# Optimization experiments

Measured on AMD Instinct MI355X. Metric: run time of the kernel, lower is better.

Reference implementation:

```python
import jax, jax.numpy as jnp
import numpy as np

B, T, NCH, NBIN, NBAND = 2, 400, 8, 512, 40
NPV = NCH * NCH


def setup_inputs() -> dict:
    key = jax.random.key(0)
    ks = jax.random.split(key, 7)
    bins_real = jax.random.normal(ks[0], (B, T, NCH, NBIN), jnp.float32)
    bins_imag = jax.random.normal(ks[1], (B, T, NCH, NBIN), jnp.float32)
    band_matrix_real = jax.random.normal(ks[2], (NBIN, NBAND), jnp.float32) * 0.05
    band_matrix_imag = jax.random.normal(ks[3], (NBIN, NBAND), jnp.float32) * 0.05
    cov_to_pv_real = jax.random.normal(ks[4], (NPV, NCH * NCH), jnp.float32) * 0.1
    cov_to_pv_imag = jax.random.normal(ks[5], (NPV, NCH * NCH), jnp.float32) * 0.1
    tau = jax.random.uniform(ks[6], (NBAND,), jnp.float32, 0.8, 0.99)
    return {
        'bins_real': bins_real, 'bins_imag': bins_imag,
        'band_matrix_real': band_matrix_real, 'band_matrix_imag': band_matrix_imag,
        'cov_to_pv_real': cov_to_pv_real, 'cov_to_pv_imag': cov_to_pv_imag,
        'tau': tau,
    }


def _power_vector(bins_real, bins_imag, band_matrix_real, band_matrix_imag,
                  cov_to_pv_real, cov_to_pv_imag, tau):
    x = jax.lax.complex(bins_real, bins_imag)            # (B,T,C,F)
    nch = x.shape[-2]
    EPS = 1e-20
    # per-bin covariance outer product, flattened cov dim: (B,T,F,C*C)
    cov = jnp.einsum('btif,btjf->btfij', x, jnp.conj(x))
    b, t, f = cov.shape[:3]
    cov = cov.reshape(b, t, f, nch * nch)
    diag = jnp.arange(nch) * (nch + 1)                   # diagonal indices in cov dim
    trace = jnp.clip(jnp.sum(cov.real[..., diag], axis=-1, keepdims=True), EPS, None)
    cov = cov / trace                                    # per-bin trace normalisation
    # phase adjustment along the bin axis (n=1 -> lag of 2 bins)
    c = jnp.swapaxes(cov, -1, -2)                        # (B,T,C2,F)
    prod = jnp.conj(c[..., :-2]) * c[..., 2:]
    ang = jnp.arctan2(prod.imag, prod.real)
    ang = jnp.concatenate([ang[..., :1], ang, ang[..., -1:]], axis=-1)  # edge pad
    adj = jnp.abs(c) * jax.lax.complex(jnp.cos(ang), jnp.sin(ang))
    adj = adj.at[..., diag, :].set(c[..., diag, :])      # keep original diagonals
    # band projection: contract bins against (F,K) band matrix
    bm = jax.lax.complex(band_matrix_real, band_matrix_imag)
    band_cov = jnp.einsum('btcf,fk->btkc', adj, bm)      # (B,T,K,C2)
    dsum = jnp.clip(band_cov.real[..., diag].sum(-1, keepdims=True), EPS, None)
    band_cov = band_cov / dsum
    # first-order IIR smoothing over frames, per-band pole tau
    a = tau[:, None].astype(band_cov.real.dtype)         # (K,1)
    def step(carry, xt):
        y = a * carry + (1.0 - a) * xt
        return y, y
    y0 = jnp.zeros_like(band_cov[:, 0])                  # (B,K,C2)
    _, ys = jax.lax.scan(step, y0, jnp.moveaxis(band_cov, 1, 0))
    band_cov = jnp.moveaxis(ys, 0, 1)                    # (B,T,K,C2)
    # cov -> power vector projection, real part
    c2p = jax.lax.complex(cov_to_pv_real, cov_to_pv_imag)  # (P,C2)
    pv = jnp.einsum('pc,btkc->btkp', c2p, band_cov).real   # (B,T,K,P)
    return pv


def reference(bins_real, bins_imag, band_matrix_real, band_matrix_imag,
              cov_to_pv_real, cov_to_pv_imag, tau):
    return _power_vector(bins_real, bins_imag, band_matrix_real, band_matrix_imag,
                         cov_to_pv_real, cov_to_pv_imag, tau)
```

## Files before the change

### kernel.cpp

```cpp
#include <hip/hip_runtime.h>

#define B_    2
#define T_    400
#define NCH_  8
#define NBIN_ 512
#define NBAND_ 40
#define NPV_  64

using short8  = __attribute__((ext_vector_type(8))) short;
using float4v = __attribute__((ext_vector_type(4))) float;

static __device__ inline unsigned pkbf(float x, float y) {
  union { float f; unsigned u; } a, b;
  a.f = x; b.f = y;
  unsigned ra = a.u + 0x7fffu + ((a.u >> 16) & 1u);
  unsigned rb = b.u + 0x7fffu + ((b.u >> 16) & 1u);
  return (ra >> 16) | (rb & 0xffff0000u);
}
static __device__ inline void upk(unsigned u, float& lo, float& hi) {
  union { unsigned q; float f; } a, b;
  a.q = u << 16; b.q = u & 0xffff0000u;
  lo = a.f; hi = b.f;
}
static __device__ inline unsigned swapvar(unsigned u) {
  unsigned r = u ^ 0x80000000u;
  return (r >> 16) | (r << 16);
}
static __device__ inline void gld_lds16(const uint4* g, uint4* l) {
  auto* lds_ptr = reinterpret_cast<__attribute__((address_space(3))) uint4*>(
      reinterpret_cast<uintptr_t>(l));
  auto* g_ptr = reinterpret_cast<const __attribute__((address_space(1))) uint4*>(
      reinterpret_cast<uintptr_t>(g));
  __builtin_amdgcn_global_load_lds(g_ptr, lds_ptr, 16, 0, 0);
}

__global__ __launch_bounds__(256) void pv_prep(
    const float* __restrict__ bmr, const float* __restrict__ bmi,
    const float* __restrict__ c2pr, const float* __restrict__ c2pi,
    float* __restrict__ ws)
{
  const int tid = threadIdx.x;
  const int blk = blockIdx.x;
  if (blk == 0) {
    __shared__ float sds[256];
    int k = tid & 63, part = tid >> 6;
    float s = 0.f;
    if (k < NBAND_) {
      const float* col = bmr + k;
      #pragma unroll 16
      for (int f = part * 128; f < part * 128 + 128; f++) s += col[f * 40];
    }
    sds[tid] = s;
    __syncthreads();
    if (tid < NBAND_) {
      float t = sds[tid] + sds[tid + 64] + sds[tid + 128] + sds[tid + 192];
      ws[tid] = 1.0f / fmaxf(t, 1e-20f);
    }
  } else if (blk <= 24) {
    int F = (blk - 1) * 256 + tid;
    int l = F & 63;
    int fid = F >> 6;
    int s5 = fid / 3;
    int n = fid - s5 * 3;
    int k = n * 16 + (l & 15);
    int quad = l >> 4;
    unsigned dw[4];
    #pragma unroll
    for (int t2 = 0; t2 < 4; t2++) {
      float v0 = 0.f, v1 = 0.f;
      if (k < NBAND_) {
        int f = s5 * 16 + quad * 4 + t2;
        v0 = bmr[f * 40 + k]; v1 = bmi[f * 40 + k];
      }
      dw[t2] = pkbf(v0, v1);
    }
    ((uint4*)((char*)ws + 1024))[F] = make_uint4(dw[0], dw[1], dw[2], dw[3]);
  } else {
    int F2 = (blk - 25) * 256 + tid;
    int lane = F2 & 63, E = F2 >> 6;
    int nt = E >> 2, ks = E & 3;
    int n = lane & 15, quad = lane >> 4;
    int p = nt * 16 + n;
    unsigned dw[4];
    #pragma unroll
    for (int t2 = 0; t2 < 4; t2++) {
      int c = ks * 16 + quad * 4 + t2;
      dw[t2] = pkbf(c2pr[p * 64 + c], -c2pi[p * 64 + c]);
    }
    ((uint4*)((char*)ws + 197632))[E * 64 + lane] = make_uint4(dw[0], dw[1], dw[2], dw[3]);
  }
}

__global__ __launch_bounds__(256, 4) void pv_main(
    const float* __restrict__ br, const float* __restrict__ bi,
    const float* __restrict__ ws, float* __restrict__ out)
{
  __shared__ __align__(16) unsigned smem[10240];
  unsigned* vsh = smem;
  uint4*    bst = (uint4*)(smem + 4096);

  const int bt  = blockIdx.x;
  const int tid = threadIdx.x;
  const float* pr  = br + (size_t)bt * (NCH_ * NBIN_);
  const float* pim = bi + (size_t)bt * (NCH_ * NBIN_);

  const int mt   = tid >> 6;
  const int lane = tid & 63;
  const int m16  = lane & 15;
  const int quad = lane >> 4;
  const int p    = mt * 16 + m16;
  const int ich  = p >> 3, jch = p & 7;
  const uint4* BF0 = (const uint4*)((const char*)ws + 1024);

  {
    const uint4* g = BF0 + tid;
    uint4* l = bst + tid;
    gld_lds16(g, l);
    gld_lds16(g + 256, l + 256);
    gld_lds16(g + 512, l + 512);
  }

  #pragma unroll
  for (int fs = 0; fs < 2; fs++) {
    const int f = fs * 256 + tid;
    const int fm = (f == 0) ? 0 : ((f == 511) ? 509 : f - 1);
    const int fp = (f == 0) ? 2 : ((f == 511) ? 511 : f + 1);
    float tr = 0.f;
    float t1[8], t2[8];
    #pragma unroll
    for (int c = 0; c < 8; c++) {
      const float* cr = pr + c * 512;
      const float* ci = pim + c * 512;
      float xr = cr[f],   xi = ci[f];
      float xrm = cr[fm], xim = ci[fm];
      float xrp = cr[fp], xip = ci[fp];
      tr = fmaf(xr, xr, tr); tr = fmaf(xi, xi, tr);
      float Gr = fmaf(xrm, xrp,  xim * xip);
      float Gi = fmaf(xrm, xip, -(xim * xrp));
      float am = fmaxf(fmaxf(fabsf(Gr), fabsf(Gi)), 1e-30f);
      float rc = __builtin_amdgcn_rcpf(am);
      float q1 = Gr * rc, q2 = Gi * rc;
      float n2 = fmaf(q1, q1, q2 * q2);
      float rn = __builtin_amdgcn_rsqf(n2);
      bool ok = n2 > 0.f;
      float ur = ok ? q1 * rn : 1.f;
      float ui = ok ? q2 * rn : 0.f;
      float mg = __builtin_amdgcn_sqrtf(fmaf(xr, xr, xi * xi));
      t1[c] = mg * ur; t2[c] = mg * ui;
    }
    float scv = __builtin_amdgcn_rsqf(fmaxf(tr, 1e-20f));
    #pragma unroll
    for (int c = 0; c < 8; c++)
      vsh[c * 512 + f] = pkbf(t1[c] * scv, t2[c] * scv);
  }
  __syncthreads();

  const uint4* Avp = (const uint4*)(vsh + ich * 512) + quad;
  const uint4* Bvp = (const uint4*)(vsh + jch * 512) + quad;

  float4v acc[6];
  #pragma unroll
  for (int g = 0; g < 6; g++) acc[g] = (float4v){0.f, 0.f, 0.f, 0.f};

  for (int st = 0; st < 8; st++) {
    if (st < 7) {
      const uint4* g = BF0 + (st + 1) * 768 + tid;
      uint4* l = bst + ((st + 1) & 1) * 768 + tid;
      gld_lds16(g, l);
      gld_lds16(g + 256, l + 256);
      gld_lds16(g + 512, l + 512);
    }
    const uint4* bb = bst + (st & 1) * 768;
    #pragma unroll
    for (int q = 0; q < 4; q++) {
      const int s = st * 4 + q;
      uint4 av = Avp[s * 4];
      uint4 bv = Bvp[s * 4];
      uint4 cb0 = bb[(q * 3 + 0) * 64 + lane];
      uint4 cb1 = bb[(q * 3 + 1) * 64 + lane];
      uint4 cb2 = bb[(q * 3 + 2) * 64 + lane];
      float ar[4], ai[4];
      {
        float vr, vi, wr, wi;
        upk(av.x, vr, vi); upk(bv.x, wr, wi);
        ar[0] = fmaf(vr, wr,  vi * wi); ai[0] = fmaf(vi, wr, -(vr * wi));
        upk(av.y, vr, vi); upk(bv.y, wr, wi);
        ar[1] = fmaf(vr, wr,  vi * wi); ai[1] = fmaf(vi, wr, -(vr * wi));
        upk(av.z, vr, vi); upk(bv.z, wr, wi);
        ar[2] = fmaf(vr, wr,  vi * wi); ai[2] = fmaf(vi, wr, -(vr * wi));
        upk(av.w, vr, vi); upk(bv.w, wr, wi);
        ar[3] = fmaf(vr, wr,  vi * wi); ai[3] = fmaf(vi, wr, -(vr * wi));
      }
      uint4 au1 = make_uint4(pkbf(ar[0], -ai[0]), pkbf(ar[1], -ai[1]),
                             pkbf(ar[2], -ai[2]), pkbf(ar[3], -ai[3]));
      uint4 au2 = make_uint4(swapvar(au1.x), swapvar(au1.y),
                             swapvar(au1.z), swapvar(au1.w));
      short8 af1 = __builtin_bit_cast(short8, au1);
      short8 af2 = __builtin_bit_cast(short8, au2);
      short8 b0 = __builtin_bit_cast(short8, cb0);
      short8 b1 = __builtin_bit_cast(short8, cb1);
      short8 b2 = __builtin_bit_cast(short8, cb2);
      acc[0] = __builtin_amdgcn_mfma_f32_16x16x32_bf16(af1, b0, acc[0], 0, 0, 0);
      acc[3] = __builtin_amdgcn_mfma_f32_16x16x32_bf16(af2, b0, acc[3], 0, 0, 0);
      acc[1] = __builtin_amdgcn_mfma_f32_16x16x32_bf16(af1, b1, acc[1], 0, 0, 0);
      acc[4] = __builtin_amdgcn_mfma_f32_16x16x32_bf16(af2, b1, acc[4], 0, 0, 0);
      acc[2] = __builtin_amdgcn_mfma_f32_16x16x32_bf16(af1, b2, acc[2], 0, 0, 0);
      acc[5] = __builtin_amdgcn_mfma_f32_16x16x32_bf16(af2, b2, acc[5], 0, 0, 0);
    }
    __syncthreads();
  }

  const uint4* EF = ((const uint4*)((const char*)ws + 197632)) + (mt * 4) * 64 + lane;
  uint4 eb[4];
  #pragma unroll
  for (int ks = 0; ks < 4; ks++) eb[ks] = EF[ks * 64];

  unsigned* bcsh = smem;
  #pragma unroll
  for (int n = 0; n < 3; n++) {
    uint4 w4 = make_uint4(pkbf(acc[n][0], acc[n + 3][0]),
                          pkbf(acc[n][1], acc[n + 3][1]),
                          pkbf(acc[n][2], acc[n + 3][2]),
                          pkbf(acc[n][3], acc[n + 3][3]));
    *(uint4*)(bcsh + (n * 16 + m16) * 68 + mt * 16 + quad * 4) = w4;
  }
  __syncthreads();

  float4v eacc[3];
  #pragma unroll
  for (int kt = 0; kt < 3; kt++) eacc[kt] = (float4v){0.f, 0.f, 0.f, 0.f};
  #pragma unroll
  for (int ks = 0; ks < 4; ks++) {
    short8 bfr = __builtin_bit_cast(short8, eb[ks]);
    #pragma unroll
    for (int kt = 0; kt < 3; kt++) {
      uint4 a4 = *(const uint4*)(bcsh + (kt * 16 + m16) * 68 + ks * 16 + quad * 4);
      short8 afr = __builtin_bit_cast(short8, a4);
      eacc[kt] = __builtin_amdgcn_mfma_f32_16x16x32_bf16(afr, bfr, eacc[kt], 0, 0, 0);
    }
  }
  float* op = out + (size_t)bt * (NBAND_ * NPV_);
  const float4* wsd = (const float4*)ws;
  #pragma unroll
  for (int kt = 0; kt < 3; kt++) {
    float4 dv = wsd[kt * 4 + quad];
    float dva[4] = {dv.x, dv.y, dv.z, dv.w};
    #pragma unroll
    for (int r = 0; r < 4; r++) {
      int k = kt * 16 + quad * 4 + r;
      if (k < NBAND_)
        op[k * 64 + mt * 16 + m16] = eacc[kt][r] * dva[r];
    }
  }
}

__global__ __launch_bounds__(256) void pv_iir3(float* __restrict__ z,
                                               const float* __restrict__ tau)
{
  __shared__ float gsh[16][16];
  const int pg = blockIdx.x & 3;
  const int bk = blockIdx.x >> 2;
  const int k = bk % NBAND_;
  const int b = bk / NBAND_;
  const float a  = tau[k];
  const float om = 1.0f - a;
  const int c  = threadIdx.x >> 4;
  const int pl = threadIdx.x & 15;
  const int p  = pg * 16 + pl;
  const size_t stride = (size_t)NBAND_ * 64;
  size_t idx0 = (size_t)b * (T_ * NBAND_ * 64) + (size_t)(c * 25) * stride + k * 64 + p;

  float y[25];
  float accv = 0.f;
  #pragma unroll
  for (int i = 0; i < 25; i++) {
    float v = z[idx0 + (size_t)i * stride];
    accv = fmaf(a, accv, om * v);
    y[i] = accv;
  }
  gsh[c][pl] = accv;
  __syncthreads();
  float a2 = a * a, a8 = a2 * a2 * a2 * a2, a16 = a8 * a8;
  float A = a16 * a8 * a;
  float H = 0.f;
  #pragma unroll
  for (int d = 0; d < 15; d++) {
    if (d < c) H = fmaf(A, H, gsh[d][pl]);
  }
  float wp = a;
  #pragma unroll
  for (int i = 0; i < 25; i++) {
    z[idx0 + (size_t)i * stride] = fmaf(wp, H, y[i]);
    wp *= a;
  }
}

extern "C" void kernel_launch(void* const* d_in, const int* in_sizes, int n_in,
                              void* d_out, int out_size, void* d_ws, size_t ws_size,
                              hipStream_t stream)
{
  const float* br   = (const float*)d_in[0];
  const float* bi   = (const float*)d_in[1];
  const float* bmr  = (const float*)d_in[2];
  const float* bmi  = (const float*)d_in[3];
  const float* c2pr = (const float*)d_in[4];
  const float* c2pi = (const float*)d_in[5];
  const float* tau  = (const float*)d_in[6];
  float* out = (float*)d_out;
  float* ws  = (float*)d_ws;

  hipLaunchKernelGGL(pv_prep, dim3(29), dim3(256), 0, stream,
                     bmr, bmi, c2pr, c2pi, ws);
  hipLaunchKernelGGL(pv_main, dim3(B_ * T_), dim3(256), 0, stream,
                     br, bi, ws, out);
  hipLaunchKernelGGL(pv_iir3, dim3(B_ * NBAND_ * 4), dim3(256), 0, stream,
                     out, tau);
}
```

Baseline: 119.8 us.

## Switch MFMA operands to fp16 with packed half2 complex multiply and XOR-swizzled LDS

Moves every packed operand from software-rounded bf16 to fp16. The per-bin complex conjugate product is now computed with packed half2 multiply and FMA instructions, replacing the scalar unpack, fp32 FMA and repack sequence, and the MFMAs use the f16 variant. The per-channel vector stores in shared memory are XOR-swizzled by channel to reduce LDS bank conflicts when different channel rows are read. This trades bf16 range for fp16 precision and could overflow or underflow for values outside fp16 range, although trace normalisation keeps the magnitudes bounded.

```diff
diff --git a/kernel.cpp b/kernel.cpp
--- a/kernel.cpp
+++ b/kernel.cpp
@@ -1,4 +1,5 @@
 #include <hip/hip_runtime.h>
+#include <hip/hip_fp16.h>
 
 #define B_    2
 #define T_    400
@@ -7,24 +8,24 @@
 #define NBAND_ 40
 #define NPV_  64
 
-using short8  = __attribute__((ext_vector_type(8))) short;
+using half8   = __attribute__((ext_vector_type(8))) _Float16;
 using float4v = __attribute__((ext_vector_type(4))) float;
 
-static __device__ inline unsigned pkbf(float x, float y) {
-  union { float f; unsigned u; } a, b;
-  a.f = x; b.f = y;
-  unsigned ra = a.u + 0x7fffu + ((a.u >> 16) & 1u);
-  unsigned rb = b.u + 0x7fffu + ((b.u >> 16) & 1u);
-  return (ra >> 16) | (rb & 0xffff0000u);
-}
-static __device__ inline void upk(unsigned u, float& lo, float& hi) {
-  union { unsigned q; float f; } a, b;
-  a.q = u << 16; b.q = u & 0xffff0000u;
-  lo = a.f; hi = b.f;
-}
-static __device__ inline unsigned swapvar(unsigned u) {
-  unsigned r = u ^ 0x80000000u;
-  return (r >> 16) | (r << 16);
+static __device__ inline unsigned pkhf(float x, float y) {
+  __half2 h = __float22half2_rn(make_float2(x, y));
+  return __builtin_bit_cast(unsigned, h);
+}
+static __device__ inline unsigned rot16(unsigned u) {
+  return (u >> 16) | (u << 16);
+}
+static __device__ inline unsigned cmulc(unsigned viu, unsigned vju) {
+  __half2 Vi = __builtin_bit_cast(__half2, viu);
+  __half2 Vj = __builtin_bit_cast(__half2, vju);
+  __half2 P1 = __hmul2(Vi, __low2half2(Vj));
+  __half2 Qi = __lowhigh2highlow(Vi);
+  unsigned tn = __builtin_bit_cast(unsigned, __high2half2(Vj)) ^ 0x80000000u;
+  __half2 a  = __hfma2(Qi, __builtin_bit_cast(__half2, tn), P1);
+  return __builtin_bit_cast(unsigned, a);
 }
 static __device__ inline void gld_lds16(const uint4* g, uint4* l) {
   auto* lds_ptr = reinterpret_cast<__attribute__((address_space(3))) uint4*>(
@@ -72,7 +73,7 @@
         int f = s5 * 16 + quad * 4 + t2;
         v0 = bmr[f * 40 + k]; v1 = bmi[f * 40 + k];
       }
-      dw[t2] = pkbf(v0, v1);
+      dw[t2] = pkhf(v0, v1);
     }
     ((uint4*)((char*)ws + 1024))[F] = make_uint4(dw[0], dw[1], dw[2], dw[3]);
   } else {
@@ -85,7 +86,7 @@
     #pragma unroll
     for (int t2 = 0; t2 < 4; t2++) {
       int c = ks * 16 + quad * 4 + t2;
-      dw[t2] = pkbf(c2pr[p * 64 + c], -c2pi[p * 64 + c]);
+      dw[t2] = pkhf(c2pr[p * 64 + c], -c2pi[p * 64 + c]);
     }
     ((uint4*)((char*)ws + 197632))[E * 64 + lane] = make_uint4(dw[0], dw[1], dw[2], dw[3]);
   }
@@ -149,14 +150,14 @@
       t1[c] = mg * ur; t2[c] = mg * ui;
     }
     float scv = __builtin_amdgcn_rsqf(fmaxf(tr, 1e-20f));
+    const int fc = f >> 2, fl = f & 3;
     #pragma unroll
     for (int c = 0; c < 8; c++)
-      vsh[c * 512 + f] = pkbf(t1[c] * scv, t2[c] * scv);
+      vsh[c * 512 + ((fc ^ c) << 2) + fl] = pkhf(t1[c] * scv, t2[c] * scv);
   }
   __syncthreads();
 
-  const uint4* Avp = (const uint4*)(vsh + ich * 512) + quad;
-  const uint4* Bvp = (const uint4*)(vsh + jch * 512) + quad;
+  const uint4* vb = (const uint4*)vsh;
 
   float4v acc[6];
   #pragma unroll
@@ -174,38 +175,31 @@
     #pragma unroll
     for (int q = 0; q < 4; q++) {
       const int s = st * 4 + q;
-      uint4 av = Avp[s * 4];
-      uint4 bv = Bvp[s * 4];
+      const int sc = s * 4 + quad;
+      uint4 av = vb[ich * 128 + (sc ^ ich)];
+      uint4 bv = vb[jch * 128 + (sc ^ jch)];
       uint4 cb0 = bb[(q * 3 + 0) * 64 + lane];
       uint4 cb1 = bb[(q * 3 + 1) * 64 + lane];
       uint4 cb2 = bb[(q * 3 + 2) * 64 + lane];
-      float ar[4], ai[4];
-      {
-        float vr, vi, wr, wi;
-        upk(av.x, vr, vi); upk(bv.x, wr, wi);
-        ar[0] = fmaf(vr, wr,  vi * wi); ai[0] = fmaf(vi, wr, -(vr * wi));
-        upk(av.y, vr, vi); upk(bv.y, wr, wi);
-        ar[1] = fmaf(vr, wr,  vi * wi); ai[1] = fmaf(vi, wr, -(vr * wi));
-        upk(av.z, vr, vi); upk(bv.z, wr, wi);
-        ar[2] = fmaf(vr, wr,  vi * wi); ai[2] = fmaf(vi, wr, -(vr * wi));
-        upk(av.w, vr, vi); upk(bv.w, wr, wi);
-        ar[3] = fmaf(vr, wr,  vi * wi); ai[3] = fmaf(vi, wr, -(vr * wi));
-      }
-      uint4 au1 = make_uint4(pkbf(ar[0], -ai[0]), pkbf(ar[1], -ai[1]),
-                             pkbf(ar[2], -ai[2]), pkbf(ar[3], -ai[3]));
-      uint4 au2 = make_uint4(swapvar(au1.x), swapvar(au1.y),
-                             swapvar(au1.z), swapvar(au1.w));
-      short8 af1 = __builtin_bit_cast(short8, au1);
-      short8 af2 = __builtin_bit_cast(short8, au2);
-      short8 b0 = __builtin_bit_cast(short8, cb0);
-      short8 b1 = __builtin_bit_cast(short8, cb1);
-      short8 b2 = __builtin_bit_cast(short8, cb2);
-      acc[0] = __builtin_amdgcn_mfma_f32_16x16x32_bf16(af1, b0, acc[0], 0, 0, 0);
-      acc[3] = __builtin_amdgcn_mfma_f32_16x16x32_bf16(af2, b0, acc[3], 0, 0, 0);
-      acc[1] = __builtin_amdgcn_mfma_f32_16x16x32_bf16(af1, b1, acc[1], 0, 0, 0);
-      acc[4] = __builtin_amdgcn_mfma_f32_16x16x32_bf16(af2, b1, acc[4], 0, 0, 0);
-      acc[2] = __builtin_amdgcn_mfma_f32_16x16x32_bf16(af1, b2, acc[2], 0, 0, 0);
-      acc[5] = __builtin_amdgcn_mfma_f32_16x16x32_bf16(af2, b2, acc[5], 0, 0, 0);
+      unsigned a0 = cmulc(av.x, bv.x);
+      unsigned a1 = cmulc(av.y, bv.y);
+      unsigned a2 = cmulc(av.z, bv.z);
+      unsigned a3 = cmulc(av.w, bv.w);
+      uint4 au1 = make_uint4(a0 ^ 0x80000000u, a1 ^ 0x80000000u,
+                             a2 ^ 0x80000000u, a3 ^ 0x80000000u);
+      uint4 au2 = make_uint4(rot16(a0), rot16(a1),
+                             rot16(a2), rot16(a3));
+      half8 af1 = __builtin_bit_cast(half8, au1);
+      half8 af2 = __builtin_bit_cast(half8, au2);
+      half8 b0 = __builtin_bit_cast(half8, cb0);
+      half8 b1 = __builtin_bit_cast(half8, cb1);
+      half8 b2 = __builtin_bit_cast(half8, cb2);
+      acc[0] = __builtin_amdgcn_mfma_f32_16x16x32_f16(af1, b0, acc[0], 0, 0, 0);
+      acc[3] = __builtin_amdgcn_mfma_f32_16x16x32_f16(af2, b0, acc[3], 0, 0, 0);
+      acc[1] = __builtin_amdgcn_mfma_f32_16x16x32_f16(af1, b1, acc[1], 0, 0, 0);
+      acc[4] = __builtin_amdgcn_mfma_f32_16x16x32_f16(af2, b1, acc[4], 0, 0, 0);
+      acc[2] = __builtin_amdgcn_mfma_f32_16x16x32_f16(af1, b2, acc[2], 0, 0, 0);
+      acc[5] = __builtin_amdgcn_mfma_f32_16x16x32_f16(af2, b2, acc[5], 0, 0, 0);
     }
     __syncthreads();
   }
@@ -218,10 +212,10 @@
   unsigned* bcsh = smem;
   #pragma unroll
   for (int n = 0; n < 3; n++) {
-    uint4 w4 = make_uint4(pkbf(acc[n][0], acc[n + 3][0]),
-                          pkbf(acc[n][1], acc[n + 3][1]),
-                          pkbf(acc[n][2], acc[n + 3][2]),
-                          pkbf(acc[n][3], acc[n + 3][3]));
+    uint4 w4 = make_uint4(pkhf(acc[n][0], acc[n + 3][0]),
+                          pkhf(acc[n][1], acc[n + 3][1]),
+                          pkhf(acc[n][2], acc[n + 3][2]),
+                          pkhf(acc[n][3], acc[n + 3][3]));
     *(uint4*)(bcsh + (n * 16 + m16) * 68 + mt * 16 + quad * 4) = w4;
   }
   __syncthreads();
@@ -231,12 +225,12 @@
   for (int kt = 0; kt < 3; kt++) eacc[kt] = (float4v){0.f, 0.f, 0.f, 0.f};
   #pragma unroll
   for (int ks = 0; ks < 4; ks++) {
-    short8 bfr = __builtin_bit_cast(short8, eb[ks]);
+    half8 bfr = __builtin_bit_cast(half8, eb[ks]);
     #pragma unroll
     for (int kt = 0; kt < 3; kt++) {
       uint4 a4 = *(const uint4*)(bcsh + (kt * 16 + m16) * 68 + ks * 16 + quad * 4);
-      short8 afr = __builtin_bit_cast(short8, a4);
-      eacc[kt] = __builtin_amdgcn_mfma_f32_16x16x32_bf16(afr, bfr, eacc[kt], 0, 0, 0);
+      half8 afr = __builtin_bit_cast(half8, a4);
+      eacc[kt] = __builtin_amdgcn_mfma_f32_16x16x32_f16(afr, bfr, eacc[kt], 0, 0, 0);
     }
   }
   float* op = out + (size_t)bt * (NBAND_ * NPV_);
```

After: 114.0 us. -4.8%, faster.
